# Kernel tuning notes

Measured on AMD Instinct MI355X. Metric: run time of the kernel, lower is better.

Reference implementation:

```python
import jax, jax.numpy as jnp
import numpy as np

NEG_SLOPE = 0.2  # both GATConv internal LeakyReLU and the module-level activation


def gat_conv(x, src, dst, W, a_src, a_dst, bias):
    """PyG GATConv (concat=True, add_self_loops handled by caller via src/dst).
    x: [N, Din]; W: [Din, H*C]; a_src, a_dst: [H, C]; bias: [H*C]."""
    N = x.shape[0]
    H, C = a_src.shape
    h = (x @ W).reshape(N, H, C)                       # [N, H, C]
    al_src = jnp.einsum('nhc,hc->nh', h, a_src)        # [N, H]
    al_dst = jnp.einsum('nhc,hc->nh', h, a_dst)        # [N, H]
    e = jax.nn.leaky_relu(al_src[src] + al_dst[dst], NEG_SLOPE)  # [E, H]
    # segment softmax over edges grouped by destination node
    m = jax.ops.segment_max(e, dst, num_segments=N)    # [N, H]
    ex = jnp.exp(e - m[dst])
    denom = jax.ops.segment_sum(ex, dst, num_segments=N)
    alpha = ex / denom[dst]                            # [E, H]
    out = jax.ops.segment_sum(alpha[:, :, None] * h[src], dst, num_segments=N)
    return out.reshape(N, H * C) + bias


def setup_inputs() -> dict:
    key = jax.random.key(0)
    N, E = 50000, 800000
    D_IN, HID, H = 128, 128, 2
    C = HID // H
    ks = jax.random.split(key, 20)
    inp = {
        'x': jax.random.normal(ks[0], (N, D_IN), dtype=jnp.float32),
        'edge_index': jax.random.randint(ks[1], (2, E), 0, N, dtype=jnp.int64),
    }
    dims = [D_IN, HID, HID]  # input dims of the 3 GATConv layers
    for i, din in enumerate(dims, start=1):
        s = 1.0 / np.sqrt(din)
        inp[f'W{i}'] = jax.random.normal(ks[2 + 4 * i], (din, HID), dtype=jnp.float32) * s
        inp[f'a_src{i}'] = jax.random.normal(ks[3 + 4 * i], (H, C), dtype=jnp.float32) * 0.1
        inp[f'a_dst{i}'] = jax.random.normal(ks[4 + 4 * i], (H, C), dtype=jnp.float32) * 0.1
        inp[f'b{i}'] = jnp.zeros((HID,), dtype=jnp.float32)
    inp['lin_w'] = jax.random.normal(ks[2], (HID, 1), dtype=jnp.float32) * (1.0 / np.sqrt(HID))
    inp['lin_b'] = jnp.zeros((1,), dtype=jnp.float32)
    return inp


def reference(x, edge_index, W1, a_src1, a_dst1, b1, W2, a_src2, a_dst2, b2,
              W3, a_src3, a_dst3, b3, lin_w, lin_b):
    N = x.shape[0]
    loops = jnp.arange(N, dtype=edge_index.dtype)
    src = jnp.concatenate([edge_index[0], loops])  # add_self_loops=True
    dst = jnp.concatenate([edge_index[1], loops])

    h = jax.nn.leaky_relu(gat_conv(x, src, dst, W1, a_src1, a_dst1, b1), NEG_SLOPE)
    # dropout is identity in eval mode (p=0.0)
    h = jax.nn.leaky_relu(h + gat_conv(h, src, dst, W2, a_src2, a_dst2, b2), NEG_SLOPE)
    h = jax.nn.leaky_relu(h + gat_conv(h, src, dst, W3, a_src3, a_dst3, b3), NEG_SLOPE)
    logits = (h @ lin_w + lin_b).squeeze(-1)  # [N]
    return logits
```

## Files before the change

### kernel.cpp

```cpp
#include <hip/hip_runtime.h>
#include <hip/hip_bf16.h>
#include <hip/hip_fp16.h>

#define LEAK 0.2f

typedef _Float16 half8  __attribute__((ext_vector_type(8)));
typedef _Float16 half4v __attribute__((ext_vector_type(4)));
typedef float    float4v __attribute__((ext_vector_type(4)));


__global__ __launch_bounds__(256) void k_bincount(const int* __restrict__ edst,
                                                  int* __restrict__ gbkt,
                                                  int E, int ETOT, int NBK) {
    __shared__ int lh[512];
    int t = threadIdx.x;
    for (int b = t; b < NBK; b += 256) lh[b] = 0;
    __syncthreads();
    int base = blockIdx.x * 4096;
    #pragma unroll
    for (int u = 0; u < 16; ++u) {
        int e = base + u * 256 + t;
        if (e < ETOT) {
            int d = (e < E) ? edst[e] : (e - E);
            atomicAdd(&lh[d >> 7], 1);
        }
    }
    __syncthreads();
    for (int b = t; b < NBK; b += 256)
        if (lh[b]) atomicAdd(&gbkt[b], lh[b]);
}

__global__ __launch_bounds__(512) void k_bktscan(const int* __restrict__ gbkt,
                                                 int* __restrict__ bko,
                                                 int* __restrict__ gcur, int NBK) {
    int t = threadIdx.x;
    int v = (t < NBK) ? gbkt[t] : 0;
    int lane = t & 63, wid = t >> 6;
    int x = v;
    #pragma unroll
    for (int o = 1; o < 64; o <<= 1) {
        int y = __shfl_up(x, o);
        if (lane >= o) x += y;
    }
    __shared__ int ws[8];
    if (lane == 63) ws[wid] = x;
    __syncthreads();
    if (wid == 0) {
        int s = (lane < 8) ? ws[lane] : 0;
        #pragma unroll
        for (int o = 1; o < 8; o <<= 1) {
            int y = __shfl_up(s, o);
            if (lane >= o) s += y;
        }
        if (lane < 8) ws[lane] = s;
    }
    __syncthreads();
    int excl = x - v + (wid > 0 ? ws[wid - 1] : 0);
    if (t < NBK) { bko[t] = excl; gcur[t] = excl; }
    if (t == 511) bko[NBK] = excl;
}

__global__ __launch_bounds__(256) void k_binscatter(const int* __restrict__ esrc,
                                                    const int* __restrict__ edst,
                                                    int* __restrict__ gcur,
                                                    unsigned int* __restrict__ binned,
                                                    int E, int ETOT, int NBK) {
    __shared__ int lh[512];
    __shared__ int lbase[512];
    int t = threadIdx.x;
    for (int b = t; b < NBK; b += 256) lh[b] = 0;
    __syncthreads();
    int base = blockIdx.x * 4096;
    unsigned int word[16]; int bb[16], rk[16];
    #pragma unroll
    for (int u = 0; u < 16; ++u) {
        int e = base + u * 256 + t;
        bb[u] = -1;
        if (e < ETOT) {
            int s, d;
            if (e < E) { s = esrc[e]; d = edst[e]; } else { s = d = e - E; }
            int b = d >> 7;
            bb[u] = b;
            rk[u] = atomicAdd(&lh[b], 1);
            word[u] = (unsigned int)s | ((unsigned int)(d & 127) << 17);
        }
    }
    __syncthreads();
    for (int b = t; b < NBK; b += 256) {
        int c = lh[b];
        lbase[b] = c ? atomicAdd(&gcur[b], c) : 0;
    }
    __syncthreads();
    #pragma unroll
    for (int u = 0; u < 16; ++u)
        if (bb[u] >= 0) binned[lbase[bb[u]] + rk[u]] = word[u];
}

__global__ __launch_bounds__(256) void k_scatter2(const unsigned int* __restrict__ binned,
                                                  const int* __restrict__ bko,
                                                  int* __restrict__ off,
                                                  int* __restrict__ csr, int N, int NBK) {
    __shared__ int deg[128];
    __shared__ int lcur[128];
    __shared__ int wt[2];
    int b = blockIdx.x, t = threadIdx.x;
    int n0 = b << 7;
    if (t < 128) deg[t] = 0;
    __syncthreads();
    int beg = bko[b], end = bko[b + 1];
    for (int i = beg + t; i < end; i += 256)
        atomicAdd(&deg[binned[i] >> 17], 1);
    __syncthreads();
    int v = 0, x = 0;
    if (t < 128) {
        v = deg[t];
        x = v;
        int lane = t & 63;
        #pragma unroll
        for (int o = 1; o < 64; o <<= 1) {
            int y = __shfl_up(x, o);
            if (lane >= o) x += y;
        }
        if (lane == 63) wt[t >> 6] = x;
    }
    __syncthreads();
    if (t < 128) {
        int excl = x - v + ((t >= 64) ? wt[0] : 0) + beg;
        lcur[t] = excl;
        int node = n0 + t;
        if (node < N) off[node] = excl;
    }
    if (b == NBK - 1 && t == 0) off[N] = end;
    __syncthreads();
    for (int i = beg + t; i < end; i += 256) {
        unsigned int u = binned[i];
        int pos = atomicAdd(&lcur[u >> 17], 1);
        csr[pos] = (int)(u & 0x1FFFF);
    }
}


__global__ __launch_bounds__(256) void k_wconv(const float* __restrict__ W0,
                                               const float* __restrict__ W1,
                                               const float* __restrict__ W2,
                                               _Float16* __restrict__ w16) {
    int i = blockIdx.x * 256 + threadIdx.x;
    if (i >= 3 * 16384) return;
    const float* src = (i < 16384) ? W0 : (i < 32768 ? W1 : W2);
    w16[i] = (_Float16)src[i & 16383];
}


__global__ __launch_bounds__(256) void k_gemm_mfma(const float* __restrict__ X,
                                                   const _Float16* __restrict__ Wh,
                                                   const float* __restrict__ a_src,
                                                   const float* __restrict__ a_dst,
                                                   _Float16* __restrict__ Hout,
                                                   float* __restrict__ alsrc,
                                                   float* __restrict__ aldst, int N) {
    __shared__ _Float16 As[64][136];
    __shared__ float sS[64][2];
    __shared__ float sD[64][2];
    const int t = threadIdx.x;
    const int lane = t & 63, w = t >> 6;
    const int block_row = blockIdx.x * 64;

    if (t < 128) { sS[t >> 1][t & 1] = 0.f; sD[t >> 1][t & 1] = 0.f; }

    #pragma unroll
    for (int it = 0; it < 8; ++it) {
        int i = t + 256 * it;
        int row = i >> 5, c4 = i & 31;
        int gr = block_row + row;
        float4 xv = make_float4(0.f, 0.f, 0.f, 0.f);
        if (gr < N) xv = *(const float4*)(X + (size_t)gr * 128 + c4 * 4);
        half4v hv;
        hv[0] = (_Float16)xv.x; hv[1] = (_Float16)xv.y;
        hv[2] = (_Float16)xv.z; hv[3] = (_Float16)xv.w;
        *(half4v*)(&As[row][c4 * 4]) = hv;
    }

    const int l15 = lane & 15, kq = (lane >> 4) * 8;
    half8 bf[2][4];
    #pragma unroll
    for (int ntl = 0; ntl < 2; ++ntl) {
        int n0 = (w * 2 + ntl) * 16 + l15;
        #pragma unroll
        for (int kt = 0; kt < 4; ++kt)
            #pragma unroll
            for (int j = 0; j < 8; ++j)
                bf[ntl][kt][j] = Wh[(kt * 32 + kq + j) * 128 + n0];
    }
    __syncthreads();

    float4v acc[4][2];
    #pragma unroll
    for (int mt = 0; mt < 4; ++mt)
        #pragma unroll
        for (int ntl = 0; ntl < 2; ++ntl)
            acc[mt][ntl] = (float4v){0.f, 0.f, 0.f, 0.f};

    #pragma unroll
    for (int kt = 0; kt < 4; ++kt) {
        half8 a[4];
        #pragma unroll
        for (int mt = 0; mt < 4; ++mt)
            a[mt] = *(const half8*)(&As[mt * 16 + l15][kt * 32 + kq]);
        #pragma unroll
        for (int mt = 0; mt < 4; ++mt)
            #pragma unroll
            for (int ntl = 0; ntl < 2; ++ntl)
                acc[mt][ntl] = __builtin_amdgcn_mfma_f32_16x16x32_f16(
                    a[mt], bf[ntl][kt], acc[mt][ntl], 0, 0, 0);
    }

    #pragma unroll
    for (int mt = 0; mt < 4; ++mt) {
        int r0 = block_row + mt * 16 + (lane >> 4) * 4;
        #pragma unroll
        for (int ntl = 0; ntl < 2; ++ntl) {
            int col = (w * 2 + ntl) * 16 + l15;
            #pragma unroll
            for (int reg = 0; reg < 4; ++reg) {
                int r = r0 + reg;
                if (r < N) Hout[(size_t)r * 128 + col] = (_Float16)acc[mt][ntl][reg];
            }
        }
    }

    {
        int c0 = w * 32 + l15, c1 = c0 + 16;
        float as0 = a_src[c0], as1 = a_src[c1];
        float ad0 = a_dst[c0], ad1 = a_dst[c1];
        int head = w >> 1;
        #pragma unroll
        for (int mt = 0; mt < 4; ++mt) {
            #pragma unroll
            for (int reg = 0; reg < 4; ++reg) {
                float ps = (float)acc[mt][0][reg] * as0 + (float)acc[mt][1][reg] * as1;
                float pd = (float)acc[mt][0][reg] * ad0 + (float)acc[mt][1][reg] * ad1;
                #pragma unroll
                for (int o = 1; o < 16; o <<= 1) {
                    ps += __shfl_xor(ps, o);
                    pd += __shfl_xor(pd, o);
                }
                if (l15 == 0) {
                    int row = mt * 16 + (lane >> 4) * 4 + reg;
                    atomicAdd(&sS[row][head], ps);
                    atomicAdd(&sD[row][head], pd);
                }
            }
        }
    }
    __syncthreads();
    if (t < 128) {
        int row = t >> 1, head = t & 1;
        int gr = block_row + row;
        if (gr < N) {
            alsrc[gr * 2 + head] = sS[row][head];
            aldst[gr * 2 + head] = sD[row][head];
        }
    }
}


__global__ __launch_bounds__(256) void k_aggregate(
        const _Float16* __restrict__ H16,
        const float* __restrict__ alsrc,
        const float* __restrict__ aldst,
        const int* __restrict__ off, const int* __restrict__ csr,
        const float* __restrict__ bias,
        const float* __restrict__ prev,
        float* __restrict__ Out,
        const float* __restrict__ lw, const float* __restrict__ lb,
        float* __restrict__ logits, int N, int mode) {
    int node = (int)((blockIdx.x * 256 + threadIdx.x) >> 6);
    int lane = threadIdx.x & 63;
    if (node >= N) return;
    int beg = off[node], end = off[node + 1];
    float ad0 = aldst[node * 2], ad1 = aldst[node * 2 + 1];

    int p = lane & 15;
    int q = lane >> 4;
    bool head0 = p < 8;
    const _Float16* hbase = H16 + p * 8;

    float acc[8];
    #pragma unroll
    for (int i = 0; i < 8; ++i) acc[i] = 0.f;
    float dsum = 0.f;

    for (int base = beg; base < end; base += 64) {
        int i = base + lane;
        float w0 = 0.f, w1 = 0.f; int s = 0;
        if (i < end) {
            s = csr[i];
            float2 al = *(const float2*)(&alsrc[s * 2]);
            float e0 = al.x + ad0; e0 = e0 > 0.f ? e0 : LEAK * e0;
            float e1 = al.y + ad1; e1 = e1 > 0.f ? e1 : LEAK * e1;
            w0 = __expf(e0); w1 = __expf(e1);
        }
        int cnt = min(64, end - base);
        int iters = (cnt + 3) >> 2;
        int jj = 0;
        for (; jj + 2 <= iters; jj += 2) {
            int sl0 = (jj << 2) + q, sl1 = sl0 + 4;
            int   sj0  = __shfl(s,  sl0);
            float w0j0 = __shfl(w0, sl0);
            float w1j0 = __shfl(w1, sl0);
            int   sj1  = __shfl(s,  sl1);
            float w0j1 = __shfl(w0, sl1);
            float w1j1 = __shfl(w1, sl1);
            float wsel0 = head0 ? w0j0 : w1j0;
            float wsel1 = head0 ? w0j1 : w1j1;
            uint4 raw0 = *(const uint4*)(hbase + (size_t)sj0 * 128);
            uint4 raw1 = *(const uint4*)(hbase + (size_t)sj1 * 128);
            const _Float16* h0 = (const _Float16*)&raw0;
            const _Float16* h1 = (const _Float16*)&raw1;
            #pragma unroll
            for (int k = 0; k < 8; ++k) acc[k] += wsel0 * (float)h0[k];
            #pragma unroll
            for (int k = 0; k < 8; ++k) acc[k] += wsel1 * (float)h1[k];
            dsum += wsel0 + wsel1;
        }
        if (jj < iters) {
            int sl = (jj << 2) + q;
            int   sj  = __shfl(s,  sl);
            float w0j = __shfl(w0, sl);
            float w1j = __shfl(w1, sl);
            float wsel = head0 ? w0j : w1j;
            uint4 raw = *(const uint4*)(hbase + (size_t)sj * 128);
            const _Float16* h = (const _Float16*)&raw;
            #pragma unroll
            for (int k = 0; k < 8; ++k) acc[k] += wsel * (float)h[k];
            dsum += wsel;
        }
    }

    #pragma unroll
    for (int i = 0; i < 8; ++i) {
        acc[i] += __shfl_xor(acc[i], 16);
        acc[i] += __shfl_xor(acc[i], 32);
    }
    dsum += __shfl_xor(dsum, 16);
    dsum += __shfl_xor(dsum, 32);

    if (q == 0) {
        float inv = 1.f / dsum;
        int c0 = p * 8;
        float v[8];
        #pragma unroll
        for (int i = 0; i < 8; ++i) v[i] = acc[i] * inv + bias[c0 + i];
        if (mode >= 1) {
            float4 p0 = *(const float4*)(&prev[(size_t)node * 128 + c0]);
            float4 p1 = *(const float4*)(&prev[(size_t)node * 128 + c0 + 4]);
            v[0] += p0.x; v[1] += p0.y; v[2] += p0.z; v[3] += p0.w;
            v[4] += p1.x; v[5] += p1.y; v[6] += p1.z; v[7] += p1.w;
        }
        #pragma unroll
        for (int i = 0; i < 8; ++i) v[i] = v[i] > 0.f ? v[i] : LEAK * v[i];
        if (mode == 2) {
            float partial = 0.f;
            #pragma unroll
            for (int i = 0; i < 8; ++i) partial += v[i] * lw[c0 + i];
            partial += __shfl_xor(partial, 1);
            partial += __shfl_xor(partial, 2);
            partial += __shfl_xor(partial, 4);
            partial += __shfl_xor(partial, 8);
            if (p == 0) logits[node] = partial + lb[0];
        } else {
            *(float4*)(&Out[(size_t)node * 128 + c0])     = make_float4(v[0], v[1], v[2], v[3]);
            *(float4*)(&Out[(size_t)node * 128 + c0 + 4]) = make_float4(v[4], v[5], v[6], v[7]);
        }
    }
}


extern "C" void kernel_launch(void* const* d_in, const int* in_sizes, int n_in,
                              void* d_out, int out_size, void* d_ws, size_t ws_size,
                              hipStream_t stream) {
    const float* x    = (const float*)d_in[0];
    const int*   edge = (const int*)d_in[1];
    const float* W[3]  = {(const float*)d_in[2], (const float*)d_in[6], (const float*)d_in[10]};
    const float* as[3] = {(const float*)d_in[3], (const float*)d_in[7], (const float*)d_in[11]};
    const float* ad[3] = {(const float*)d_in[4], (const float*)d_in[8], (const float*)d_in[12]};
    const float* bs[3] = {(const float*)d_in[5], (const float*)d_in[9], (const float*)d_in[13]};
    const float* lw = (const float*)d_in[14];
    const float* lb = (const float*)d_in[15];

    const int N    = in_sizes[0] / 128;
    const int E    = in_sizes[1] / 2;
    const int ETOT = E + N;
    const int NBK  = (N + 127) >> 7;

    char* base = (char*)d_ws;
    size_t o = 0;
    auto carve = [&](size_t bytes) {
        char* p = base + o;
        o = (o + bytes + 255) & ~(size_t)255;
        return p;
    };
    int*      off    = (int*)     carve((size_t)(N + 1) * 4);
    int*      gbkt   = (int*)     carve((size_t)(NBK + 1) * 4);
    int*      bko    = (int*)     carve((size_t)(NBK + 1) * 4);
    int*      gcur   = (int*)     carve((size_t)(NBK + 1) * 4);
    unsigned* binned = (unsigned*)carve((size_t)ETOT * 4);
    int*      csr    = (int*)     carve((size_t)ETOT * 4);
    float*    alsrc  = (float*)   carve((size_t)N * 2 * 4);
    float*    aldst  = (float*)   carve((size_t)N * 2 * 4);
    _Float16* h16    = (_Float16*)carve((size_t)N * 128 * 2);
    float*    bufA   = (float*)   carve((size_t)N * 128 * 4);
    float*    bufB   = (float*)   carve((size_t)N * 128 * 4);
    _Float16* w16    = (_Float16*)carve((size_t)3 * 16384 * 2);
    (void)ws_size; (void)n_in; (void)out_size;

    const int* esrc = edge;
    const int* edst = edge + E;

    int eb = (ETOT + 4095) / 4096;

    hipMemsetAsync(gbkt, 0, (size_t)(NBK + 1) * 4, stream);
    k_wconv<<<192, 256, 0, stream>>>(W[0], W[1], W[2], w16);

    k_bincount<<<eb, 256, 0, stream>>>(edst, gbkt, E, ETOT, NBK);
    k_bktscan<<<1, 512, 0, stream>>>(gbkt, bko, gcur, NBK);
    k_binscatter<<<eb, 256, 0, stream>>>(esrc, edst, gcur, binned, E, ETOT, NBK);
    k_scatter2<<<NBK, 256, 0, stream>>>(binned, bko, off, csr, N, NBK);

    int gemm_blocks = (N + 63) / 64;
    int node_blocks = (N * 64 + 255) / 256;

    k_gemm_mfma<<<gemm_blocks, 256, 0, stream>>>(x, w16, as[0], ad[0], h16, alsrc, aldst, N);
    k_aggregate<<<node_blocks, 256, 0, stream>>>(h16, alsrc, aldst, off, csr,
                                                 bs[0], nullptr, bufA, lw, lb, nullptr, N, 0);
    k_gemm_mfma<<<gemm_blocks, 256, 0, stream>>>(bufA, w16 + 16384, as[1], ad[1], h16, alsrc, aldst, N);
    k_aggregate<<<node_blocks, 256, 0, stream>>>(h16, alsrc, aldst, off, csr,
                                                 bs[1], bufA, bufB, lw, lb, nullptr, N, 1);
    k_gemm_mfma<<<gemm_blocks, 256, 0, stream>>>(bufB, w16 + 32768, as[2], ad[2], h16, alsrc, aldst, N);
    k_aggregate<<<node_blocks, 256, 0, stream>>>(h16, alsrc, aldst, off, csr,
                                                 bs[2], bufB, nullptr, lw, lb, (float*)d_out, N, 2);
}
```

Measured before the change: 302.2 us.

## Pack two destination nodes per wavefront in aggregation and pre-transpose weights

Result: faster. 290.2 us (-4.0%).

```diff
diff --git a/kernel.cpp b/kernel.cpp
--- a/kernel.cpp
+++ b/kernel.cpp
@@ -143,16 +143,27 @@
 __global__ __launch_bounds__(256) void k_wconv(const float* __restrict__ W0,
                                                const float* __restrict__ W1,
                                                const float* __restrict__ W2,
-                                               _Float16* __restrict__ w16) {
-    int i = blockIdx.x * 256 + threadIdx.x;
-    if (i >= 3 * 16384) return;
-    const float* src = (i < 16384) ? W0 : (i < 32768 ? W1 : W2);
-    w16[i] = (_Float16)src[i & 16383];
+                                               _Float16* __restrict__ w16t) {
+    __shared__ _Float16 tile[64][68];
+    int m = blockIdx.x >> 2;
+    int ti = (blockIdx.x >> 1) & 1, tj = blockIdx.x & 1;
+    const float* src = (m == 0) ? W0 : (m == 1 ? W1 : W2);
+    _Float16* dst = w16t + m * 16384;
+    int t = threadIdx.x;
+    for (int idx = t; idx < 4096; idx += 256) {
+        int r = idx >> 6, c = idx & 63;
+        tile[r][c] = (_Float16)src[(ti * 64 + r) * 128 + tj * 64 + c];
+    }
+    __syncthreads();
+    for (int idx = t; idx < 4096; idx += 256) {
+        int c = idx >> 6, r = idx & 63;
+        dst[(tj * 64 + c) * 128 + ti * 64 + r] = tile[r][c];
+    }
 }
 
 
 __global__ __launch_bounds__(256) void k_gemm_mfma(const float* __restrict__ X,
-                                                   const _Float16* __restrict__ Wh,
+                                                   const _Float16* __restrict__ WhT,
                                                    const float* __restrict__ a_src,
                                                    const float* __restrict__ a_dst,
                                                    _Float16* __restrict__ Hout,
@@ -187,9 +198,7 @@
         int n0 = (w * 2 + ntl) * 16 + l15;
         #pragma unroll
         for (int kt = 0; kt < 4; ++kt)
-            #pragma unroll
-            for (int j = 0; j < 8; ++j)
-                bf[ntl][kt][j] = Wh[(kt * 32 + kq + j) * 128 + n0];
+            bf[ntl][kt] = *(const half8*)(WhT + (size_t)n0 * 128 + kt * 32 + kq);
     }
     __syncthreads();
 
@@ -274,25 +283,32 @@
         float* __restrict__ Out,
         const float* __restrict__ lw, const float* __restrict__ lb,
         float* __restrict__ logits, int N, int mode) {
-    int node = (int)((blockIdx.x * 256 + threadIdx.x) >> 6);
+    int wglobal = (int)((blockIdx.x * 256 + threadIdx.x) >> 6);
     int lane = threadIdx.x & 63;
-    if (node >= N) return;
-    int beg = off[node], end = off[node + 1];
-    float ad0 = aldst[node * 2], ad1 = aldst[node * 2 + 1];
-
-    int p = lane & 15;
-    int q = lane >> 4;
+    if (wglobal * 2 >= N) return;
+    int half = lane >> 5;
+    int hl = lane & 31;
+    int node = wglobal * 2 + half;
+    bool active = node < N;
+    int nodeC = active ? node : (N - 1);
+    int beg = off[nodeC];
+    int end = active ? off[nodeC + 1] : beg;
+    float ad0 = aldst[nodeC * 2], ad1 = aldst[nodeC * 2 + 1];
+
+    int p = hl & 15;
+    int q = hl >> 4;
     bool head0 = p < 8;
     const _Float16* hbase = H16 + p * 8;
+    int hb = half << 5;
 
     float acc[8];
     #pragma unroll
-    for (int i = 0; i < 8; ++i) acc[i] = 0.f;
+    for (int k = 0; k < 8; ++k) acc[k] = 0.f;
     float dsum = 0.f;
 
-    for (int base = beg; base < end; base += 64) {
-        int i = base + lane;
-        float w0 = 0.f, w1 = 0.f; int s = 0;
+    for (int base = beg; base < end; base += 32) {
+        int i = base + hl;
+        int s = 0; float w0 = 0.f, w1 = 0.f;
         if (i < end) {
             s = csr[i];
             float2 al = *(const float2*)(&alsrc[s * 2]);
@@ -300,57 +316,54 @@
             float e1 = al.y + ad1; e1 = e1 > 0.f ? e1 : LEAK * e1;
             w0 = __expf(e0); w1 = __expf(e1);
         }
-        int cnt = min(64, end - base);
-        int iters = (cnt + 3) >> 2;
+        int cnt = min(32, end - base);
+        int iters = (cnt + 1) >> 1;
         int jj = 0;
         for (; jj + 2 <= iters; jj += 2) {
-            int sl0 = (jj << 2) + q, sl1 = sl0 + 4;
-            int   sj0  = __shfl(s,  sl0);
-            float w0j0 = __shfl(w0, sl0);
-            float w1j0 = __shfl(w1, sl0);
-            int   sj1  = __shfl(s,  sl1);
-            float w0j1 = __shfl(w0, sl1);
-            float w1j1 = __shfl(w1, sl1);
-            float wsel0 = head0 ? w0j0 : w1j0;
-            float wsel1 = head0 ? w0j1 : w1j1;
+            int sl0 = hb + (jj << 1) + q;
+            int sl1 = sl0 + 2;
+            int   sj0 = __shfl(s,  sl0);
+            float w00 = __shfl(w0, sl0);
+            float w10 = __shfl(w1, sl0);
+            int   sj1 = __shfl(s,  sl1);
+            float w01 = __shfl(w0, sl1);
+            float w11 = __shfl(w1, sl1);
+            float ws0 = head0 ? w00 : w10;
+            float ws1 = head0 ? w01 : w11;
             uint4 raw0 = *(const uint4*)(hbase + (size_t)sj0 * 128);
             uint4 raw1 = *(const uint4*)(hbase + (size_t)sj1 * 128);
             const _Float16* h0 = (const _Float16*)&raw0;
             const _Float16* h1 = (const _Float16*)&raw1;
             #pragma unroll
-            for (int k = 0; k < 8; ++k) acc[k] += wsel0 * (float)h0[k];
-            #pragma unroll
-            for (int k = 0; k < 8; ++k) acc[k] += wsel1 * (float)h1[k];
-            dsum += wsel0 + wsel1;
+            for (int k = 0; k < 8; ++k) acc[k] += ws0 * (float)h0[k];
+            #pragma unroll
+            for (int k = 0; k < 8; ++k) acc[k] += ws1 * (float)h1[k];
+            dsum += ws0 + ws1;
         }
         if (jj < iters) {
-            int sl = (jj << 2) + q;
-            int   sj  = __shfl(s,  sl);
-            float w0j = __shfl(w0, sl);
-            float w1j = __shfl(w1, sl);
-            float wsel = head0 ? w0j : w1j;
+            int sl = hb + (jj << 1) + q;
+            int   sj = __shfl(s,  sl);
+            float wa = __shfl(w0, sl);
+            float wb = __shfl(w1, sl);
+            float ws = head0 ? wa : wb;
             uint4 raw = *(const uint4*)(hbase + (size_t)sj * 128);
             const _Float16* h = (const _Float16*)&raw;
             #pragma unroll
-            for (int k = 0; k < 8; ++k) acc[k] += wsel * (float)h[k];
-            dsum += wsel;
-        }
-    }
-
-    #pragma unroll
-    for (int i = 0; i < 8; ++i) {
-        acc[i] += __shfl_xor(acc[i], 16);
-        acc[i] += __shfl_xor(acc[i], 32);
-    }
+            for (int k = 0; k < 8; ++k) acc[k] += ws * (float)h[k];
+            dsum += ws;
+        }
+    }
+
+    #pragma unroll
+    for (int k = 0; k < 8; ++k) acc[k] += __shfl_xor(acc[k], 16);
     dsum += __shfl_xor(dsum, 16);
-    dsum += __shfl_xor(dsum, 32);
-
-    if (q == 0) {
+
+    if (q == 0 && active) {
         float inv = 1.f / dsum;
         int c0 = p * 8;
         float v[8];
         #pragma unroll
-        for (int i = 0; i < 8; ++i) v[i] = acc[i] * inv + bias[c0 + i];
+        for (int k = 0; k < 8; ++k) v[k] = acc[k] * inv + bias[c0 + k];
         if (mode >= 1) {
             float4 p0 = *(const float4*)(&prev[(size_t)node * 128 + c0]);
             float4 p1 = *(const float4*)(&prev[(size_t)node * 128 + c0 + 4]);
@@ -358,16 +371,16 @@
             v[4] += p1.x; v[5] += p1.y; v[6] += p1.z; v[7] += p1.w;
         }
         #pragma unroll
-        for (int i = 0; i < 8; ++i) v[i] = v[i] > 0.f ? v[i] : LEAK * v[i];
+        for (int k = 0; k < 8; ++k) v[k] = v[k] > 0.f ? v[k] : LEAK * v[k];
         if (mode == 2) {
             float partial = 0.f;
             #pragma unroll
-            for (int i = 0; i < 8; ++i) partial += v[i] * lw[c0 + i];
+            for (int k = 0; k < 8; ++k) partial += v[k] * lw[c0 + k];
             partial += __shfl_xor(partial, 1);
             partial += __shfl_xor(partial, 2);
             partial += __shfl_xor(partial, 4);
             partial += __shfl_xor(partial, 8);
-            if (p == 0) logits[node] = partial + lb[0];
+            if (hl == 0) logits[node] = partial + lb[0];
         } else {
             *(float4*)(&Out[(size_t)node * 128 + c0])     = make_float4(v[0], v[1], v[2], v[3]);
             *(float4*)(&Out[(size_t)node * 128 + c0 + 4]) = make_float4(v[4], v[5], v[6], v[7]);
@@ -411,7 +424,7 @@
     _Float16* h16    = (_Float16*)carve((size_t)N * 128 * 2);
     float*    bufA   = (float*)   carve((size_t)N * 128 * 4);
     float*    bufB   = (float*)   carve((size_t)N * 128 * 4);
-    _Float16* w16    = (_Float16*)carve((size_t)3 * 16384 * 2);
+    _Float16* w16t   = (_Float16*)carve((size_t)3 * 16384 * 2);
     (void)ws_size; (void)n_in; (void)out_size;
 
     const int* esrc = edge;
@@ -420,7 +433,7 @@
     int eb = (ETOT + 4095) / 4096;
 
     hipMemsetAsync(gbkt, 0, (size_t)(NBK + 1) * 4, stream);
-    k_wconv<<<192, 256, 0, stream>>>(W[0], W[1], W[2], w16);
+    k_wconv<<<12, 256, 0, stream>>>(W[0], W[1], W[2], w16t);
 
     k_bincount<<<eb, 256, 0, stream>>>(edst, gbkt, E, ETOT, NBK);
     k_bktscan<<<1, 512, 0, stream>>>(gbkt, bko, gcur, NBK);
@@ -428,15 +441,15 @@
     k_scatter2<<<NBK, 256, 0, stream>>>(binned, bko, off, csr, N, NBK);
 
     int gemm_blocks = (N + 63) / 64;
-    int node_blocks = (N * 64 + 255) / 256;
-
-    k_gemm_mfma<<<gemm_blocks, 256, 0, stream>>>(x, w16, as[0], ad[0], h16, alsrc, aldst, N);
-    k_aggregate<<<node_blocks, 256, 0, stream>>>(h16, alsrc, aldst, off, csr,
-                                                 bs[0], nullptr, bufA, lw, lb, nullptr, N, 0);
-    k_gemm_mfma<<<gemm_blocks, 256, 0, stream>>>(bufA, w16 + 16384, as[1], ad[1], h16, alsrc, aldst, N);
-    k_aggregate<<<node_blocks, 256, 0, stream>>>(h16, alsrc, aldst, off, csr,
-                                                 bs[1], bufA, bufB, lw, lb, nullptr, N, 1);
-    k_gemm_mfma<<<gemm_blocks, 256, 0, stream>>>(bufB, w16 + 32768, as[2], ad[2], h16, alsrc, aldst, N);
-    k_aggregate<<<node_blocks, 256, 0, stream>>>(h16, alsrc, aldst, off, csr,
-                                                 bs[2], bufB, nullptr, lw, lb, (float*)d_out, N, 2);
-}
+    int agg_blocks  = (N + 7) / 8;
+
+    k_gemm_mfma<<<gemm_blocks, 256, 0, stream>>>(x, w16t, as[0], ad[0], h16, alsrc, aldst, N);
+    k_aggregate<<<agg_blocks, 256, 0, stream>>>(h16, alsrc, aldst, off, csr,
+                                                bs[0], nullptr, bufA, lw, lb, nullptr, N, 0);
+    k_gemm_mfma<<<gemm_blocks, 256, 0, stream>>>(bufA, w16t + 16384, as[1], ad[1], h16, alsrc, aldst, N);
+    k_aggregate<<<agg_blocks, 256, 0, stream>>>(h16, alsrc, aldst, off, csr,
+                                                bs[1], bufA, bufB, lw, lb, nullptr, N, 1);
+    k_gemm_mfma<<<gemm_blocks, 256, 0, stream>>>(bufB, w16t + 32768, as[2], ad[2], h16, alsrc, aldst, N);
+    k_aggregate<<<agg_blocks, 256, 0, stream>>>(h16, alsrc, aldst, off, csr,
+                                                bs[2], bufB, nullptr, lw, lb, (float*)d_out, N, 2);
+}
```
